# Performance work log

Hardware: AMD Instinct MI355X
Metric: run time of the kernel (lower is better)

Reference implementation:

```python
import jax, jax.numpy as jnp
import numpy as np

B, S, D, H = 2, 2048, 1024, 16
DK = D // H


def setup_inputs() -> dict:
    key = jax.random.key(0)
    ks = jax.random.split(key, 7)
    scale = 1.0 / np.sqrt(D)
    return {
        "q": jax.random.normal(ks[0], (B, S, D), dtype=jnp.float32),
        "k": jax.random.normal(ks[1], (B, S, D), dtype=jnp.float32),
        "v": jax.random.normal(ks[2], (B, S, D), dtype=jnp.float32),
        "mask": jnp.ones((B, 1, 1, S), dtype=jnp.int32),
        "Wq": (jax.random.normal(ks[3], (D, D), dtype=jnp.float32) * scale),
        "Wk": (jax.random.normal(ks[4], (D, D), dtype=jnp.float32) * scale),
        "Wv": (jax.random.normal(ks[5], (D, D), dtype=jnp.float32) * scale),
        "Wo": (jax.random.normal(ks[6], (D, D), dtype=jnp.float32) * scale),
    }


def reference(q, k, v, mask, Wq, Wk, Wv, Wo):
    # nn.Linear(bias=False): y = x @ W.T
    def split_heads(x):  # [B,S,D] -> [B,H,S,DK]
        return x.reshape(B, S, H, DK).transpose(0, 2, 1, 3)

    qh = split_heads(q @ Wq.T)
    kh = split_heads(k @ Wk.T)
    vh = split_heads(v @ Wv.T)

    scores = jnp.einsum("bhqd,bhkd->bhqk", qh, kh) / jnp.sqrt(
        jnp.asarray(DK, dtype=qh.dtype))
    scores = jnp.where(mask == 0, jnp.asarray(-1e9, dtype=scores.dtype), scores)
    attn = jax.nn.softmax(scores, axis=-1)  # dropout p=0.0 -> identity

    ctx = jnp.einsum("bhqk,bhkd->bhqd", attn, vh)  # [B,H,S,DK]
    ctx = ctx.transpose(0, 2, 1, 3).reshape(B, S, D)
    return ctx @ Wo.T
```

## Files before the change

kernel.cpp:

```cpp
#include <hip/hip_runtime.h>


typedef __bf16 bf16x8 __attribute__((ext_vector_type(8)));
typedef __bf16 bf16x4 __attribute__((ext_vector_type(4)));
typedef float f32x4 __attribute__((ext_vector_type(4)));

#define B_ 2
#define S_ 2048
#define D_ 1024
#define H_ 16
#define DK_ 64
#define QSCALE 0.18033688011112042f

__global__ void detect_dtype(const unsigned int* __restrict__ qw,
                             int* __restrict__ flag) {
  int cnt = 0;
#pragma unroll
  for (int i = 0; i < 4; ++i) {
    unsigned int w = qw[threadIdx.x + 64 * i];
    int e = (w >> 7) & 0xFF;
    cnt += (e >= 100 && e <= 140) ? 1 : 0;
  }
#pragma unroll
  for (int off = 32; off > 0; off >>= 1) cnt += __shfl_down(cnt, off, 64);
  if (threadIdx.x == 0) *flag = (cnt >= 128) ? 0 : 1;
}

__device__ __forceinline__ bf16x8 load8cvt(const void* base, size_t eoff,
                                           bool f32) {
  if (!f32) return *(const bf16x8*)((const __bf16*)base + eoff);
  const float* p = (const float*)base + eoff;
  bf16x8 r;
#pragma unroll
  for (int j = 0; j < 8; ++j) r[j] = (__bf16)p[j];
  return r;
}

__device__ __forceinline__ void async_cp16(const __bf16* g, __bf16* l) {
  __builtin_amdgcn_global_load_lds(
      (const __attribute__((address_space(1))) unsigned int*)g,
      (__attribute__((address_space(3))) unsigned int*)l, 16, 0, 0);
}

template <int MODE>
__global__ __launch_bounds__(256) void gemm3(
    const void* X0, const void* X1, const void* X2,
    const void* W0, const void* W1, const void* W2,
    void* O0, void* O1, void* O2, const int* __restrict__ dflag) {
  constexpr int Kd = 1024, Nd = 1024;
  const void* X = (blockIdx.z == 0) ? X0 : (blockIdx.z == 1 ? X1 : X2);
  const void* W = (blockIdx.z == 0) ? W0 : (blockIdx.z == 1 ? W1 : W2);
  void* O = (blockIdx.z == 0) ? O0 : (blockIdx.z == 1 ? O1 : O2);
  const bool f32io = (*dflag != 0);

  __shared__ __attribute__((aligned(16))) __bf16 As[128][40];
  __shared__ __attribute__((aligned(16))) __bf16 Bs[128][40];

  const int m0 = blockIdx.x * 128;
  const int n0 = blockIdx.y * 128;
  const int t = threadIdx.x;
  const int lane = t & 63, wave = t >> 6;
  const int wm = (wave >> 1) * 64, wn = (wave & 1) * 64;
  const int l15 = lane & 15, quad = lane >> 4;

  f32x4 acc[4][4] = {};

  for (int k0 = 0; k0 < Kd; k0 += 32) {
    __syncthreads();
#pragma unroll
    for (int i = 0; i < 2; ++i) {
      int slot = t + 256 * i;
      int row = slot >> 2, c8 = (slot & 3) * 8;
      bf16x8 xv;
      if (MODE == 0) {
        xv = load8cvt(X, (size_t)(m0 + row) * Kd + k0 + c8, f32io);
      } else {
        int gm = m0 + row, gk = k0 + c8;
        size_t off = ((((size_t)(gm >> 11) * H_ + (gk >> 6)) * S_) +
                      (gm & (S_ - 1))) * DK_ + (gk & (DK_ - 1));
        xv = *(const bf16x8*)((const __bf16*)X + off);
      }
      bf16x8 wv = load8cvt(W, (size_t)(n0 + row) * Kd + k0 + c8, f32io);
      *(bf16x8*)&As[row][c8] = xv;
      *(bf16x8*)&Bs[row][c8] = wv;
    }
    __syncthreads();

    bf16x8 af[4], bfr[4];
#pragma unroll
    for (int mi = 0; mi < 4; ++mi)
      af[mi] = *(const bf16x8*)&As[wm + mi * 16 + l15][quad * 8];
#pragma unroll
    for (int ni = 0; ni < 4; ++ni)
      bfr[ni] = *(const bf16x8*)&Bs[wn + ni * 16 + l15][quad * 8];
#pragma unroll
    for (int mi = 0; mi < 4; ++mi)
#pragma unroll
      for (int ni = 0; ni < 4; ++ni)
        acc[mi][ni] = __builtin_amdgcn_mfma_f32_16x16x32_bf16(af[mi], bfr[ni],
                                                              acc[mi][ni], 0, 0, 0);
  }

  const float oscale = (MODE == 0 && blockIdx.z == 0) ? QSCALE : 1.0f;
#pragma unroll
  for (int mi = 0; mi < 4; ++mi) {
#pragma unroll
    for (int ni = 0; ni < 4; ++ni) {
      int mbase = m0 + wm + mi * 16 + quad * 4;
      int n = n0 + wn + ni * 16 + l15;
      if (MODE == 0 && blockIdx.z == 2) {
        int b = mbase >> 11, sb = mbase & (S_ - 1);
        int h = n >> 6, dk = n & (DK_ - 1);
        bf16x4 pk;
#pragma unroll
        for (int r = 0; r < 4; ++r) pk[r] = (__bf16)acc[mi][ni][r];
        *(bf16x4*)&((__bf16*)O)[((size_t)(b * H_ + h) * DK_ + dk) * S_ + sb] = pk;
      } else {
#pragma unroll
        for (int r = 0; r < 4; ++r) {
          int m = mbase + r;
          float val = acc[mi][ni][r] * oscale;
          if (MODE == 0) {
            int b = m >> 11, s = m & (S_ - 1);
            int h = n >> 6, dk = n & (DK_ - 1);
            ((__bf16*)O)[((size_t)(b * H_ + h) * S_ + s) * DK_ + dk] = (__bf16)val;
          } else {
            size_t idx = (size_t)m * Nd + n;
            if (f32io) ((float*)O)[idx] = val;
            else       ((__bf16*)O)[idx] = (__bf16)val;
          }
        }
      }
    }
  }
}

__global__ __launch_bounds__(256) void attn(
    const __bf16* Qh, const __bf16* __restrict__ Kh,
    const __bf16* __restrict__ Vt, const int* __restrict__ mask,
    __bf16* Out) {
  __shared__ __attribute__((aligned(16))) __bf16 Ks[2][4096];
  __shared__ __attribute__((aligned(16))) __bf16 Vs[2][4096];
  __shared__ __attribute__((aligned(16))) __bf16 P[4][2048];

  const int t = threadIdx.x;
  const int lane = t & 63, wave = t >> 6;
  const int l15 = lane & 15, quad = lane >> 4;
  const int qb = blockIdx.x & 15;
  const int bh = blockIdx.x >> 4;
  const int b = bh >> 4;
  const int q0 = qb * 128 + wave * 32;

  const __bf16* Q = Qh + (size_t)bh * S_ * DK_;
  const __bf16* K = Kh + (size_t)bh * S_ * DK_;
  const __bf16* V = Vt + (size_t)bh * DK_ * S_;
  const int* mk = mask + b * S_;

  bf16x8 qf[2][2];
#pragma unroll
  for (int qt = 0; qt < 2; ++qt)
#pragma unroll
    for (int h = 0; h < 2; ++h)
      qf[qt][h] = *(const bf16x8*)&Q[(size_t)(q0 + qt * 16 + l15) * DK_ +
                                     h * 32 + quad * 8];

  f32x4 o[2][4] = {};
  float lsum[2][4] = {};

#pragma unroll
  for (int i = 0; i < 2; ++i) {
    int l = wave * 128 + i * 64 + lane;
    int row = l >> 3, jg = (l & 7) ^ (row & 7);
    async_cp16(K + (size_t)row * DK_ + jg * 8, &Ks[0][(size_t)(l - lane) * 8]);
    async_cp16(V + (size_t)row * S_ + jg * 8, &Vs[0][(size_t)(l - lane) * 8]);
  }
  __syncthreads();

  for (int kb = 0; kb < S_; kb += 64) {
    const int cur = (kb >> 6) & 1;
    if (kb + 64 < S_) {
#pragma unroll
      for (int i = 0; i < 2; ++i) {
        int l = wave * 128 + i * 64 + lane;
        int row = l >> 3, jg = (l & 7) ^ (row & 7);
        async_cp16(K + (size_t)(kb + 64 + row) * DK_ + jg * 8,
                   &Ks[cur ^ 1][(size_t)(l - lane) * 8]);
        async_cp16(V + (size_t)row * S_ + (kb + 64) + jg * 8,
                   &Vs[cur ^ 1][(size_t)(l - lane) * 8]);
      }
    }

    const __bf16* ks = &Ks[cur][0];
    f32x4 s[2][4];
#pragma unroll
    for (int tt = 0; tt < 4; ++tt) {
      int row = tt * 16 + l15;
      bf16x8 kf0 = *(const bf16x8*)&ks[row * 64 + ((quad ^ (l15 & 7)) << 3)];
      bf16x8 kf1 = *(const bf16x8*)&ks[row * 64 + (((4 + quad) ^ (l15 & 7)) << 3)];
#pragma unroll
      for (int qt = 0; qt < 2; ++qt) {
        f32x4 z = {};
        z = __builtin_amdgcn_mfma_f32_16x16x32_bf16(qf[qt][0], kf0, z, 0, 0, 0);
        z = __builtin_amdgcn_mfma_f32_16x16x32_bf16(qf[qt][1], kf1, z, 0, 0, 0);
        s[qt][tt] = z;
      }
    }

#pragma unroll
    for (int tt = 0; tt < 4; ++tt) {
      const int mv = mk[kb + tt * 16 + l15];
      const int jbase = tt * 2 + (l15 >> 3);
      const int kl = l15 & 7;
#pragma unroll
      for (int qt = 0; qt < 2; ++qt) {
#pragma unroll
        for (int r = 0; r < 4; ++r) {
          float e = mv ? __builtin_exp2f(s[qt][tt][r]) : 0.f;
          lsum[qt][r] += e;
          int qp = qt * 16 + quad * 4 + r;
          P[wave][qp * 64 + ((jbase ^ (qp & 7)) << 3) + kl] = (__bf16)e;
        }
      }
    }

    const __bf16* vs = &Vs[cur][0];
#pragma unroll
    for (int kt = 0; kt < 2; ++kt) {
      bf16x8 pf[2];
#pragma unroll
      for (int qt = 0; qt < 2; ++qt) {
        int qp = qt * 16 + l15;
        pf[qt] = *(const bf16x8*)&P[wave][qp * 64 +
                                          (((kt * 4 + quad) ^ (l15 & 7)) << 3)];
      }
#pragma unroll
      for (int nt = 0; nt < 4; ++nt) {
        int dk = nt * 16 + l15;
        bf16x8 vf = *(const bf16x8*)&vs[dk * 64 +
                                        (((kt * 4 + quad) ^ (l15 & 7)) << 3)];
#pragma unroll
        for (int qt = 0; qt < 2; ++qt)
          o[qt][nt] = __builtin_amdgcn_mfma_f32_16x16x32_bf16(pf[qt], vf,
                                                              o[qt][nt], 0, 0, 0);
      }
    }

    __syncthreads();
  }

  float rinv[2][4];
#pragma unroll
  for (int qt = 0; qt < 2; ++qt)
#pragma unroll
    for (int r = 0; r < 4; ++r) {
      float v = lsum[qt][r];
#pragma unroll
      for (int off = 8; off > 0; off >>= 1) v += __shfl_xor(v, off, 16);
      rinv[qt][r] = 1.0f / v;
    }

#pragma unroll
  for (int qt = 0; qt < 2; ++qt)
#pragma unroll
    for (int nt = 0; nt < 4; ++nt)
#pragma unroll
      for (int r = 0; r < 4; ++r) {
        int qrow = q0 + qt * 16 + quad * 4 + r;
        Out[(size_t)bh * S_ * DK_ + (size_t)qrow * DK_ + nt * 16 + l15] =
            (__bf16)(o[qt][nt][r] * rinv[qt][r]);
      }
}

extern "C" void kernel_launch(void* const* d_in, const int* in_sizes, int n_in,
                              void* d_out, int out_size, void* d_ws, size_t ws_size,
                              hipStream_t stream) {
  const void* q = d_in[0];
  const void* k = d_in[1];
  const void* v = d_in[2];
  const int* mask = (const int*)d_in[3];
  const void* Wq = d_in[4];
  const void* Wk = d_in[5];
  const void* Wv = d_in[6];
  const void* Wo = d_in[7];

  const size_t NE = (size_t)B_ * H_ * S_ * DK_;
  __bf16* Qh = (__bf16*)d_ws;
  __bf16* Kh = Qh + NE;
  int* dflag = (int*)((char*)d_ws + 2 * NE * sizeof(__bf16));
  __bf16* Vt = (__bf16*)d_out;

  detect_dtype<<<1, 64, 0, stream>>>((const unsigned int*)q, dflag);
  dim3 g1(32, 8, 3);
  gemm3<0><<<g1, 256, 0, stream>>>(q, k, v, Wq, Wk, Wv, Qh, Kh, Vt, dflag);
  attn<<<512, 256, 0, stream>>>(Qh, Kh, Vt, mask, Qh);
  dim3 g2(32, 8, 1);
  gemm3<1><<<g2, 256, 0, stream>>>(Qh, Qh, Qh, Wo, Wo, Wo, d_out, d_out, d_out, dflag);
}
```

Baseline: 301.9 us.

## Use async global-to-LDS copies with swizzled LDS and smaller output-GEMM tiles

Generalises the GEMM kernel with a tile-height template and replaces the padded shared-memory arrays with unpadded tiles that use an XOR swizzle. When inputs are bf16, tiles are staged with direct global-to-LDS async loads, with precomputed per-lane pointers. The output projection now uses 64-row tiles, doubling its block count. With f32 inputs the async path is skipped and only the swizzled layout and new tiling apply.

New measurement: 265.6 us. 1.14x faster.

```diff
diff --git a/kernel.cpp b/kernel.cpp
--- a/kernel.cpp
+++ b/kernel.cpp
@@ -42,61 +42,116 @@
       (__attribute__((address_space(3))) unsigned int*)l, 16, 0, 0);
 }
 
-template <int MODE>
-__global__ __launch_bounds__(256) void gemm3(
+template <int TM, int MODE>
+__global__ __launch_bounds__(256) void gemmk(
     const void* X0, const void* X1, const void* X2,
     const void* W0, const void* W1, const void* W2,
     void* O0, void* O1, void* O2, const int* __restrict__ dflag) {
   constexpr int Kd = 1024, Nd = 1024;
+  constexpr int NI = (TM == 128) ? 4 : 2;
+  constexpr int ALOADS = TM / 64;
   const void* X = (blockIdx.z == 0) ? X0 : (blockIdx.z == 1 ? X1 : X2);
   const void* W = (blockIdx.z == 0) ? W0 : (blockIdx.z == 1 ? W1 : W2);
   void* O = (blockIdx.z == 0) ? O0 : (blockIdx.z == 1 ? O1 : O2);
   const bool f32io = (*dflag != 0);
 
-  __shared__ __attribute__((aligned(16))) __bf16 As[128][40];
-  __shared__ __attribute__((aligned(16))) __bf16 Bs[128][40];
-
-  const int m0 = blockIdx.x * 128;
+  __shared__ __attribute__((aligned(16))) __bf16 As[TM * 32];
+  __shared__ __attribute__((aligned(16))) __bf16 Bs[128 * 32];
+
+  const int m0 = blockIdx.x * TM;
   const int n0 = blockIdx.y * 128;
   const int t = threadIdx.x;
   const int lane = t & 63, wave = t >> 6;
-  const int wm = (wave >> 1) * 64, wn = (wave & 1) * 64;
   const int l15 = lane & 15, quad = lane >> 4;
-
-  f32x4 acc[4][4] = {};
+  const int wm = (TM == 128) ? (wave >> 1) * 64 : 0;
+  const int wn = (TM == 128) ? (wave & 1) * 64 : wave * 32;
+
+  const __bf16* gA[ALOADS];
+  __bf16* ldsA[ALOADS];
+#pragma unroll
+  for (int i = 0; i < ALOADS; ++i) {
+    int c = (wave * ALOADS + i) * 64 + lane;
+    int row = c >> 2, j = c & 3;
+    int jl = j ^ ((row >> 1) & 3);
+    ldsA[i] = &As[(wave * ALOADS + i) * 512];
+    if (MODE == 0) {
+      gA[i] = (const __bf16*)X + (size_t)(m0 + row) * Kd + jl * 8;
+    } else {
+      int gm = m0 + row;
+      gA[i] = (const __bf16*)X +
+              (size_t)(gm >> 11) * (H_ * S_ * DK_) + (size_t)(gm & (S_ - 1)) * DK_ +
+              jl * 8;
+    }
+  }
+  const __bf16* gB[2];
+  __bf16* ldsB[2];
+#pragma unroll
+  for (int i = 0; i < 2; ++i) {
+    int c = (wave * 2 + i) * 64 + lane;
+    int row = c >> 2, j = c & 3;
+    int jl = j ^ ((row >> 1) & 3);
+    ldsB[i] = &Bs[(wave * 2 + i) * 512];
+    gB[i] = (const __bf16*)W + (size_t)(n0 + row) * Kd + jl * 8;
+  }
+
+  f32x4 acc[4][NI] = {};
 
   for (int k0 = 0; k0 < Kd; k0 += 32) {
     __syncthreads();
-#pragma unroll
-    for (int i = 0; i < 2; ++i) {
-      int slot = t + 256 * i;
-      int row = slot >> 2, c8 = (slot & 3) * 8;
-      bf16x8 xv;
+    if (!f32io) {
       if (MODE == 0) {
-        xv = load8cvt(X, (size_t)(m0 + row) * Kd + k0 + c8, f32io);
+#pragma unroll
+        for (int i = 0; i < ALOADS; ++i) async_cp16(gA[i] + k0, ldsA[i]);
       } else {
-        int gm = m0 + row, gk = k0 + c8;
-        size_t off = ((((size_t)(gm >> 11) * H_ + (gk >> 6)) * S_) +
-                      (gm & (S_ - 1))) * DK_ + (gk & (DK_ - 1));
-        xv = *(const bf16x8*)((const __bf16*)X + off);
-      }
-      bf16x8 wv = load8cvt(W, (size_t)(n0 + row) * Kd + k0 + c8, f32io);
-      *(bf16x8*)&As[row][c8] = xv;
-      *(bf16x8*)&Bs[row][c8] = wv;
+        const size_t koff = (size_t)(k0 >> 6) * (S_ * DK_) + (k0 & 32);
+#pragma unroll
+        for (int i = 0; i < ALOADS; ++i) async_cp16(gA[i] + koff, ldsA[i]);
+      }
+#pragma unroll
+      for (int i = 0; i < 2; ++i) async_cp16(gB[i] + k0, ldsB[i]);
+    } else {
+#pragma unroll
+      for (int i = 0; i < TM / 64; ++i) {
+        int c = t + 256 * i;
+        int row = c >> 2, j = c & 3;
+        int jl = j ^ ((row >> 1) & 3);
+        bf16x8 xv;
+        if (MODE == 0) {
+          xv = load8cvt(X, (size_t)(m0 + row) * Kd + k0 + jl * 8, true);
+        } else {
+          int gm = m0 + row, gk = k0 + jl * 8;
+          xv = *(const bf16x8*)((const __bf16*)X +
+                ((((size_t)(gm >> 11) * H_ + (gk >> 6)) * S_) +
+                 (gm & (S_ - 1))) * DK_ + (gk & (DK_ - 1)));
+        }
+        *(bf16x8*)&As[row * 32 + j * 8] = xv;
+      }
+#pragma unroll
+      for (int i = 0; i < 2; ++i) {
+        int c = t + 256 * i;
+        int row = c >> 2, j = c & 3;
+        int jl = j ^ ((row >> 1) & 3);
+        bf16x8 wv = load8cvt(W, (size_t)(n0 + row) * Kd + k0 + jl * 8, true);
+        *(bf16x8*)&Bs[row * 32 + j * 8] = wv;
+      }
     }
     __syncthreads();
 
-    bf16x8 af[4], bfr[4];
+    bf16x8 af[4], bfr[NI];
+#pragma unroll
+    for (int mi = 0; mi < 4; ++mi) {
+      int row = wm + mi * 16 + l15;
+      af[mi] = *(const bf16x8*)&As[row * 32 + ((quad ^ ((row >> 1) & 3)) << 3)];
+    }
+#pragma unroll
+    for (int ni = 0; ni < NI; ++ni) {
+      int row = wn + ni * 16 + l15;
+      bfr[ni] = *(const bf16x8*)&Bs[row * 32 + ((quad ^ ((row >> 1) & 3)) << 3)];
+    }
 #pragma unroll
     for (int mi = 0; mi < 4; ++mi)
-      af[mi] = *(const bf16x8*)&As[wm + mi * 16 + l15][quad * 8];
-#pragma unroll
-    for (int ni = 0; ni < 4; ++ni)
-      bfr[ni] = *(const bf16x8*)&Bs[wn + ni * 16 + l15][quad * 8];
-#pragma unroll
-    for (int mi = 0; mi < 4; ++mi)
-#pragma unroll
-      for (int ni = 0; ni < 4; ++ni)
+#pragma unroll
+      for (int ni = 0; ni < NI; ++ni)
         acc[mi][ni] = __builtin_amdgcn_mfma_f32_16x16x32_bf16(af[mi], bfr[ni],
                                                               acc[mi][ni], 0, 0, 0);
   }
@@ -105,7 +160,7 @@
 #pragma unroll
   for (int mi = 0; mi < 4; ++mi) {
 #pragma unroll
-    for (int ni = 0; ni < 4; ++ni) {
+    for (int ni = 0; ni < NI; ++ni) {
       int mbase = m0 + wm + mi * 16 + quad * 4;
       int n = n0 + wn + ni * 16 + l15;
       if (MODE == 0 && blockIdx.z == 2) {
@@ -291,8 +346,9 @@
 
   detect_dtype<<<1, 64, 0, stream>>>((const unsigned int*)q, dflag);
   dim3 g1(32, 8, 3);
-  gemm3<0><<<g1, 256, 0, stream>>>(q, k, v, Wq, Wk, Wv, Qh, Kh, Vt, dflag);
+  gemmk<128, 0><<<g1, 256, 0, stream>>>(q, k, v, Wq, Wk, Wv, Qh, Kh, Vt, dflag);
   attn<<<512, 256, 0, stream>>>(Qh, Kh, Vt, mask, Qh);
-  dim3 g2(32, 8, 1);
-  gemm3<1><<<g2, 256, 0, stream>>>(Qh, Qh, Qh, Wo, Wo, Wo, d_out, d_out, d_out, dflag);
-}
+  dim3 g2(64, 8, 1);
+  gemmk<64, 1><<<g2, 256, 0, stream>>>(Qh, Qh, Qh, Wo, Wo, Wo, d_out, d_out,
+                                       d_out, dflag);
+}
```
